# Performance work log

Hardware: AMD Instinct MI355X
Metric: run time of the kernel (lower is better)

The kernel has to match this reference:

```python
import jax, jax.numpy as jnp
import numpy as np

D_MODEL, H, D_FF = 1024, 16, 4096
D_K = D_MODEL // H

def _linear_params(key, fan_in, fan_out):
    kw, kb = jax.random.split(key)
    lim = 1.0 / np.sqrt(fan_in)
    W = jax.random.uniform(kw, (fan_in, fan_out), minval=-lim, maxval=lim, dtype=jnp.float32)
    b = jax.random.uniform(kb, (fan_out,), minval=-lim, maxval=lim, dtype=jnp.float32)
    return W, b

def setup_inputs() -> dict:
    key = jax.random.key(0)
    ks = jax.random.split(key, 8)
    x = jax.random.normal(ks[0], (4, 2048, D_MODEL), dtype=jnp.float32)
    Wq, bq = _linear_params(ks[1], D_MODEL, D_MODEL)
    Wk, bk = _linear_params(ks[2], D_MODEL, D_MODEL)
    Wv, bv = _linear_params(ks[3], D_MODEL, D_MODEL)
    Wo, bo = _linear_params(ks[4], D_MODEL, D_MODEL)
    W1, b1 = _linear_params(ks[5], D_MODEL, D_FF)
    W2, b2 = _linear_params(ks[6], D_FF, D_MODEL)
    g1 = jnp.ones((D_MODEL,), jnp.float32); be1 = jnp.zeros((D_MODEL,), jnp.float32)
    g2 = jnp.ones((D_MODEL,), jnp.float32); be2 = jnp.zeros((D_MODEL,), jnp.float32)
    return {"x": x, "Wq": Wq, "bq": bq, "Wk": Wk, "bk": bk, "Wv": Wv, "bv": bv,
            "Wo": Wo, "bo": bo, "W1": W1, "b1": b1, "W2": W2, "b2": b2,
            "g1": g1, "be1": be1, "g2": g2, "be2": be2}

def _layernorm(x, g, b, eps=1e-5):
    mu = jnp.mean(x, axis=-1, keepdims=True)
    var = jnp.mean(jnp.square(x - mu), axis=-1, keepdims=True)
    return (x - mu) * jax.lax.rsqrt(var + eps) * g + b

def reference(x, Wq, bq, Wk, bk, Wv, bv, Wo, bo, W1, b1, W2, b2, g1, be1, g2, be2):
    B, S, _ = x.shape
    # project and split heads: [B, H, S, D_K]
    q = (x @ Wq + bq).reshape(B, S, H, D_K).transpose(0, 2, 1, 3)
    k = (x @ Wk + bk).reshape(B, S, H, D_K).transpose(0, 2, 1, 3)
    v = (x @ Wv + bv).reshape(B, S, H, D_K).transpose(0, 2, 1, 3)
    scores = jnp.einsum('bhqd,bhkd->bhqk', q, k) / np.sqrt(D_K).astype(np.float32)
    attn = jax.nn.softmax(scores, axis=-1)
    out = jnp.einsum('bhqk,bhkd->bhqd', attn, v)
    out = out.transpose(0, 2, 1, 3).reshape(B, S, D_MODEL)
    attn_out = out @ Wo + bo
    x1 = _layernorm(x + attn_out, g1, be1)
    ffn = jax.nn.relu(x1 @ W1 + b1) @ W2 + b2  # dropout is identity in eval
    return _layernorm(x1 + ffn, g2, be2)
```

## Files before the change

kernel.cpp:

```cpp
#include <hip/hip_runtime.h>

typedef __bf16 bf16;
typedef __bf16 bf16x4 __attribute__((ext_vector_type(4)));
typedef __bf16 bf16x8 __attribute__((ext_vector_type(8)));
typedef float  f32x4  __attribute__((ext_vector_type(4)));

#define DM   1024
#define NH   16
#define DKH  64
#define DFF  4096
#define SEQL 2048
#define NTOK 8192

typedef __attribute__((address_space(1))) void GAS;
typedef __attribute__((address_space(3))) void LAS;

__device__ inline void gload_lds16(const void* g, void* l) {
    __builtin_amdgcn_global_load_lds((GAS*)g, (LAS*)l, 16, 0, 0);
}

__global__ void cast_f32_bf16(const float* __restrict__ in, bf16* __restrict__ out, long n) {
    long i = ((long)blockIdx.x * 256 + threadIdx.x) * 4;
    long stride = (long)gridDim.x * 256 * 4;
    for (; i < n; i += stride) {
        float4 v = *(const float4*)(in + i);
        bf16x4 o = {(bf16)v.x, (bf16)v.y, (bf16)v.z, (bf16)v.w};
        *(bf16x4*)(out + i) = o;
    }
}

__global__ void transpose_cast(const float* __restrict__ src, bf16* __restrict__ dst, int R, int C) {
    __shared__ float t[32][33];
    int c0 = blockIdx.x * 32, r0 = blockIdx.y * 32;
    int tx = threadIdx.x, ty = threadIdx.y;
#pragma unroll
    for (int i = 0; i < 4; ++i)
        t[ty + i * 8][tx] = src[(long)(r0 + ty + i * 8) * C + c0 + tx];
    __syncthreads();
#pragma unroll
    for (int i = 0; i < 4; ++i)
        dst[(long)(c0 + ty + i * 8) * R + r0 + tx] = (bf16)t[tx][ty + i * 8];
}

__global__ void concat3(const float* __restrict__ a, const float* __restrict__ b,
                        const float* __restrict__ c, float* __restrict__ out) {
    int i = blockIdx.x * 256 + threadIdx.x;
    if (i < 1024) out[i] = a[i];
    else if (i < 2048) out[i] = b[i - 1024];
    else if (i < 3072) out[i] = c[i - 2048];
}

__global__ void build_vt(const bf16* __restrict__ qkv, bf16* __restrict__ vt) {
    __shared__ bf16 t[32][33];
    int bh = blockIdx.z, b = bh >> 4, h = bh & 15;
    int s0 = blockIdx.x * 32, d0 = blockIdx.y * 32;
    int tx = threadIdx.x, ty = threadIdx.y;
#pragma unroll
    for (int i = 0; i < 4; ++i)
        t[ty + i * 8][tx] = qkv[(long)(b * SEQL + s0 + ty + i * 8) * 3072 + 2 * DM + h * DKH + d0 + tx];
    __syncthreads();
#pragma unroll
    for (int i = 0; i < 4; ++i)
        vt[((long)bh * DKH + d0 + ty + i * 8) * SEQL + s0 + tx] = (bf16)t[tx][ty + i * 8];
}

__global__ __launch_bounds__(512, 2)
void gemm8p(const bf16* __restrict__ A, const bf16* __restrict__ Bt,
            const float* __restrict__ bias,
            float* __restrict__ Cf, bf16* __restrict__ Ch,
            int N, int lda, int Klen, int relu, long strideCf) {
    __shared__ bf16 As[4][4][256][8];
    __shared__ bf16 Bs[4][4][256][8];
    const int tid = threadIdx.x;
    const int lane = tid & 63;
    const int wv = tid >> 6;
    const int wr = wv >> 2, wc = wv & 3;
    const int lr = lane & 15, lg = lane >> 4;

    unsigned gx = gridDim.x, gy = gridDim.y;
    unsigned nwg = gx * gy * gridDim.z;
    unsigned wg = (blockIdx.z * gy + blockIdx.y) * gx + blockIdx.x;
    unsigned swz = (wg & 7) * (nwg >> 3) + (wg >> 3);
    unsigned bxi = swz % gx;
    unsigned rem = swz / gx;
    unsigned byi = rem % gy, bzi = rem / gy;

    const long brow = (long)byi * 256;
    const long bcol = (long)bxi * 256;
    const bf16* Ap = A + (long)bzi * Klen;
    const bf16* Bp = Bt + (long)bzi * Klen;
    float* Cfp = Cf ? Cf + (long)bzi * strideCf : nullptr;
    const float* biasp = (bzi == 0) ? bias : nullptr;

    auto stageA = [&](int X) {
        const int kt = X * 32, buf = X & 3;
#pragma unroll
        for (int j = 0; j < 2; ++j) {
            int l = j * 512 + tid;
            int kg = l >> 8, row = l & 255;
            gload_lds16(Ap + (brow + row) * (long)lda + kt + kg * 8, &As[buf][kg][row][0]);
        }
    };
    auto stageB = [&](int X) {
        const int kt = X * 32, buf = X & 3;
#pragma unroll
        for (int j = 0; j < 2; ++j) {
            int l = j * 512 + tid;
            int kg = l >> 8, row = l & 255;
            gload_lds16(Bp + (bcol + row) * (long)lda + kt + kg * 8, &Bs[buf][kg][row][0]);
        }
    };

    const int NT = Klen / 32;
    f32x4 acc[8][4] = {};

    for (int p = 0; p < 3 && p < NT; ++p) { stageA(p); stageB(p); }

    for (int T = 0; T < NT; ++T) {
        const int cur = T & 3;
        if (T + 3 < NT) stageA(T + 3);
        if (T + 3 < NT)      asm volatile("s_waitcnt vmcnt(10)" ::: "memory");
        else if (T + 2 < NT) asm volatile("s_waitcnt vmcnt(8)"  ::: "memory");
        else if (T + 1 < NT) asm volatile("s_waitcnt vmcnt(4)"  ::: "memory");
        else                 asm volatile("s_waitcnt vmcnt(0)"  ::: "memory");
        __builtin_amdgcn_s_barrier();
        asm volatile("" ::: "memory");

        bf16x8 bfv[4], af[4];
#pragma unroll
        for (int n = 0; n < 4; ++n)
            bfv[n] = *(const bf16x8*)(&Bs[cur][lg][wc * 64 + n * 16 + lr][0]);
#pragma unroll
        for (int m = 0; m < 4; ++m)
            af[m] = *(const bf16x8*)(&As[cur][lg][wr * 128 + m * 16 + lr][0]);
        asm volatile("s_waitcnt lgkmcnt(0)" ::: "memory");
        __builtin_amdgcn_sched_barrier(0);
        __builtin_amdgcn_s_setprio(1);
#pragma unroll
        for (int m = 0; m < 4; ++m)
#pragma unroll
            for (int n = 0; n < 4; ++n)
                acc[m][n] = __builtin_amdgcn_mfma_f32_16x16x32_bf16(af[m], bfv[n], acc[m][n], 0, 0, 0);
        __builtin_amdgcn_s_setprio(0);

        bf16x8 af2[4];
#pragma unroll
        for (int m = 0; m < 4; ++m)
            af2[m] = *(const bf16x8*)(&As[cur][lg][wr * 128 + (4 + m) * 16 + lr][0]);
        if (T + 3 < NT) stageB(T + 3);
        asm volatile("" ::: "memory");
        __builtin_amdgcn_s_barrier();
        asm volatile("s_waitcnt lgkmcnt(0)" ::: "memory");
        __builtin_amdgcn_sched_barrier(0);
        __builtin_amdgcn_s_setprio(1);
#pragma unroll
        for (int m = 0; m < 4; ++m)
#pragma unroll
            for (int n = 0; n < 4; ++n)
                acc[4 + m][n] = __builtin_amdgcn_mfma_f32_16x16x32_bf16(af2[m], bfv[n], acc[4 + m][n], 0, 0, 0);
        __builtin_amdgcn_s_setprio(0);
        asm volatile("" ::: "memory");
        __builtin_amdgcn_s_barrier();
    }

#pragma unroll
    for (int m = 0; m < 8; ++m) {
#pragma unroll
        for (int n = 0; n < 4; ++n) {
            long gcol = bcol + wc * 64 + n * 16 + lr;
            float bv = biasp ? biasp[gcol] : 0.f;
#pragma unroll
            for (int r = 0; r < 4; ++r) {
                long grow = brow + wr * 128 + m * 16 + lg * 4 + r;
                float v = acc[m][n][r] + bv;
                if (relu) v = v > 0.f ? v : 0.f;
                if (Cfp) Cfp[grow * N + gcol] = v;
                if (Ch) Ch[grow * N + gcol] = (bf16)v;
            }
        }
    }
}

__global__ __launch_bounds__(256, 3)
void attn_fwd(const bf16* __restrict__ qkv, const bf16* __restrict__ vt,
              bf16* __restrict__ attn_o) {
    __shared__ bf16 Ks[2][64][64];
    __shared__ bf16 Vs[2][64][64];
    __shared__ bf16 Plds[4][16][64];
    const int tid = threadIdx.x, lane = tid & 63, w = tid >> 6;
    const int lr = lane & 15, lg = lane >> 4;

    unsigned nwg = gridDim.x * gridDim.y;
    unsigned wg = blockIdx.y * gridDim.x + blockIdx.x;
    unsigned cpx = nwg >> 3;
    unsigned swzid = (wg & 7) * cpx + (wg >> 3);
    const int bx = swzid % gridDim.x, bh = swzid / gridDim.x;
    const int b = bh >> 4, h = bh & 15;
    const int q0 = bx * 128 + w * 32;

    const bf16* Q  = qkv + (long)b * SEQL * 3072 + h * DKH;
    const bf16* Kp = qkv + (long)b * SEQL * 3072 + DM + h * DKH;
    const bf16* Vp = vt + (long)bh * DKH * SEQL;

    const int r0 = w * 8 + (lane >> 3);
    const int cbb = ((lane & 7) * 16) ^ ((r0 & 7) << 4);
    const int cb = cbb >> 1;

    auto stage = [&](int buf, int j0) {
#pragma unroll
        for (int c = 0; c < 2; ++c) {
            bf16* kd = &Ks[buf][0][0] + c * 2048 + w * 512 + lane * 8;
            bf16* vd = &Vs[buf][0][0] + c * 2048 + w * 512 + lane * 8;
            gload_lds16(Kp + (long)(j0 + c * 32 + r0) * 3072 + cb, kd);
            gload_lds16(Vp + (long)(c * 32 + r0) * SEQL + j0 + cb, vd);
        }
    };

    stage(0, 0);

    bf16x8 aq[2][2];
#pragma unroll
    for (int a = 0; a < 2; ++a)
#pragma unroll
        for (int kh = 0; kh < 2; ++kh) {
            bf16x8 q = *(const bf16x8*)(Q + (long)(q0 + a * 16 + lr) * 3072 + kh * 32 + lg * 8);
#pragma unroll
            for (int e = 0; e < 8; ++e) q[e] = (bf16)((float)q[e] * 0.125f);
            aq[a][kh] = q;
        }

    float mrow[2] = {-1e30f, -1e30f};
    float lrow[2] = {0.f, 0.f};
    f32x4 accO[2][4] = {};
    char* pbase = (char*)&Plds[w][0][0];
    const int psw = (lr & 7) << 4;
    const f32x4 zero = {0.f, 0.f, 0.f, 0.f};
    int cur = 0;

    for (int it = 0; it < SEQL / 64; ++it) {
        if (it < SEQL / 64 - 1) {
            stage(cur ^ 1, (it + 1) * 64);
            asm volatile("s_waitcnt vmcnt(4)" ::: "memory");
        } else {
            asm volatile("s_waitcnt vmcnt(0)" ::: "memory");
        }
        __builtin_amdgcn_s_barrier();
        asm volatile("" ::: "memory");

        const char* Kbuf = (const char*)&Ks[cur][0][0];
        const char* Vbuf = (const char*)&Vs[cur][0][0];

        bf16x8 kf[4][2];
#pragma unroll
        for (int jh = 0; jh < 4; ++jh) {
            int row = jh * 16 + lr;
            int sw = (row & 7) << 4;
            kf[jh][0] = *(const bf16x8*)(Kbuf + row * 128 + ((lg * 16) ^ sw));
            kf[jh][1] = *(const bf16x8*)(Kbuf + row * 128 + ((64 + lg * 16) ^ sw));
        }
        bf16x8 vf[4][2];
#pragma unroll
        for (int c = 0; c < 4; ++c) {
            int row = c * 16 + lr;
            int sw = (row & 7) << 4;
            vf[c][0] = *(const bf16x8*)(Vbuf + row * 128 + ((lg * 16) ^ sw));
            vf[c][1] = *(const bf16x8*)(Vbuf + row * 128 + ((64 + lg * 16) ^ sw));
        }

#pragma unroll
        for (int a = 0; a < 2; ++a) {
            f32x4 s[4];
#pragma unroll
            for (int jh = 0; jh < 4; ++jh) {
                f32x4 t = __builtin_amdgcn_mfma_f32_16x16x32_bf16(kf[jh][0], aq[a][0], zero, 0, 0, 0);
                s[jh] = __builtin_amdgcn_mfma_f32_16x16x32_bf16(kf[jh][1], aq[a][1], t, 0, 0, 0);
            }
            float pm = s[0][0];
#pragma unroll
            for (int jh = 0; jh < 4; ++jh)
#pragma unroll
                for (int r = 0; r < 4; ++r) pm = fmaxf(pm, s[jh][r]);
            pm = fmaxf(pm, __shfl_xor(pm, 16));
            pm = fmaxf(pm, __shfl_xor(pm, 32));
            float mnew = fmaxf(mrow[a], pm);
            float al = __expf(mrow[a] - mnew);
            mrow[a] = mnew;
            float psum = 0.f;
#pragma unroll
            for (int jh = 0; jh < 4; ++jh)
#pragma unroll
                for (int r = 0; r < 4; ++r) {
                    float p = __expf(s[jh][r] - mnew);
                    s[jh][r] = p;
                    psum += p;
                }
            psum += __shfl_xor(psum, 16);
            psum += __shfl_xor(psum, 32);
            lrow[a] = lrow[a] * al + psum;
#pragma unroll
            for (int jh = 0; jh < 4; ++jh) {
                bf16x4 pw = {(bf16)s[jh][0], (bf16)s[jh][1], (bf16)s[jh][2], (bf16)s[jh][3]};
                *(bf16x4*)(pbase + lr * 128 + ((jh * 32 + lg * 8) ^ psw)) = pw;
            }
            float alr[4];
#pragma unroll
            for (int r = 0; r < 4; ++r)
                alr[r] = __shfl(al, (lane & 48) | (lg * 4 + r));
#pragma unroll
            for (int c = 0; c < 4; ++c)
#pragma unroll
                for (int r = 0; r < 4; ++r) accO[a][c][r] *= alr[r];
            bf16x8 pa[2];
#pragma unroll
            for (int i = 0; i < 2; ++i)
                pa[i] = *(const bf16x8*)(pbase + lr * 128 + ((i * 64 + lg * 16) ^ psw));
#pragma unroll
            for (int c = 0; c < 4; ++c) {
                accO[a][c] = __builtin_amdgcn_mfma_f32_16x16x32_bf16(pa[0], vf[c][0], accO[a][c], 0, 0, 0);
                accO[a][c] = __builtin_amdgcn_mfma_f32_16x16x32_bf16(pa[1], vf[c][1], accO[a][c], 0, 0, 0);
            }
        }
        asm volatile("" ::: "memory");
        __builtin_amdgcn_s_barrier();
        cur ^= 1;
    }

#pragma unroll
    for (int a = 0; a < 2; ++a) {
        float linv = 1.0f / lrow[a];
        float invr[4];
#pragma unroll
        for (int r = 0; r < 4; ++r)
            invr[r] = __shfl(linv, (lane & 48) | (lg * 4 + r));
#pragma unroll
        for (int r = 0; r < 4; ++r) {
            long grow = (long)b * SEQL + q0 + a * 16 + lg * 4 + r;
#pragma unroll
            for (int c = 0; c < 4; ++c)
                attn_o[grow * DM + h * DKH + c * 16 + lr] = (bf16)(accO[a][c][r] * invr[r]);
        }
    }
}

__global__ __launch_bounds__(256)
void add_ln(const float* __restrict__ A, const float* __restrict__ B,
            const float* __restrict__ B2,
            const float* __restrict__ g, const float* __restrict__ be,
            float* __restrict__ outf, bf16* __restrict__ outh) {
    const int w = threadIdx.x >> 6, lane = threadIdx.x & 63;
    const long row = (long)blockIdx.x * 4 + w;
    const float4* pa = (const float4*)(A + row * DM);
    const float4* pb = (const float4*)(B + row * DM);
    const float4* pb2 = B2 ? (const float4*)(B2 + row * DM) : nullptr;
    float4 v[4];
    float s = 0.f;
#pragma unroll
    for (int i = 0; i < 4; ++i) {
        float4 a = pa[i * 64 + lane], bb = pb[i * 64 + lane];
        v[i] = make_float4(a.x + bb.x, a.y + bb.y, a.z + bb.z, a.w + bb.w);
        if (pb2) {
            float4 b2 = pb2[i * 64 + lane];
            v[i].x += b2.x; v[i].y += b2.y; v[i].z += b2.z; v[i].w += b2.w;
        }
        s += v[i].x + v[i].y + v[i].z + v[i].w;
    }
#pragma unroll
    for (int off = 32; off; off >>= 1) s += __shfl_xor(s, off);
    float mu = s * (1.0f / 1024.0f);
    float var = 0.f;
#pragma unroll
    for (int i = 0; i < 4; ++i) {
        float dx = v[i].x - mu, dy = v[i].y - mu, dz = v[i].z - mu, dw = v[i].w - mu;
        var += dx * dx + dy * dy + dz * dz + dw * dw;
    }
#pragma unroll
    for (int off = 32; off; off >>= 1) var += __shfl_xor(var, off);
    float rs = 1.0f / sqrtf(var * (1.0f / 1024.0f) + 1e-5f);
    const float4* pg = (const float4*)g;
    const float4* pe = (const float4*)be;
#pragma unroll
    for (int i = 0; i < 4; ++i) {
        float4 gg = pg[i * 64 + lane], ee = pe[i * 64 + lane];
        float4 o = make_float4((v[i].x - mu) * rs * gg.x + ee.x,
                               (v[i].y - mu) * rs * gg.y + ee.y,
                               (v[i].z - mu) * rs * gg.z + ee.z,
                               (v[i].w - mu) * rs * gg.w + ee.w);
        if (outf) ((float4*)(outf + row * DM))[i * 64 + lane] = o;
        if (outh) {
            bf16x4 ho = {(bf16)o.x, (bf16)o.y, (bf16)o.z, (bf16)o.w};
            *(bf16x4*)(outh + row * DM + (i * 64 + lane) * 4) = ho;
        }
    }
}

extern "C" void kernel_launch(void* const* d_in, const int* in_sizes, int n_in,
                              void* d_out, int out_size, void* d_ws, size_t ws_size,
                              hipStream_t stream) {
    const float* x   = (const float*)d_in[0];
    const float* Wq  = (const float*)d_in[1];
    const float* bq  = (const float*)d_in[2];
    const float* Wk  = (const float*)d_in[3];
    const float* bk  = (const float*)d_in[4];
    const float* Wv  = (const float*)d_in[5];
    const float* bv  = (const float*)d_in[6];
    const float* Wo  = (const float*)d_in[7];
    const float* bo  = (const float*)d_in[8];
    const float* W1  = (const float*)d_in[9];
    const float* b1  = (const float*)d_in[10];
    const float* W2  = (const float*)d_in[11];
    const float* b2  = (const float*)d_in[12];
    const float* g1  = (const float*)d_in[13];
    const float* be1 = (const float*)d_in[14];
    const float* g2  = (const float*)d_in[15];
    const float* be2 = (const float*)d_in[16];
    float* out = (float*)d_out;

    char* ws = (char*)d_ws;
    size_t off = 0;
    auto alloc = [&](size_t bytes) {
        void* p = ws + off;
        off += (bytes + 255) & ~(size_t)255;
        return p;
    };
    bf16* xh    = (bf16*)alloc((size_t)NTOK * DM * 2);
    bf16* wqkvt = (bf16*)alloc((size_t)3072 * 1024 * 2);
    bf16* wot   = (bf16*)alloc((size_t)1024 * 1024 * 2);
    bf16* w1t   = (bf16*)alloc((size_t)4096 * 1024 * 2);
    bf16* w2t   = (bf16*)alloc((size_t)1024 * 4096 * 2);
    float* bqkv = (float*)alloc((size_t)3072 * 4);
    bf16* qkv   = (bf16*)alloc((size_t)NTOK * 3072 * 2);
    bf16* vtb   = (bf16*)alloc((size_t)NTOK * DM * 2);
    bf16* attno = (bf16*)alloc((size_t)NTOK * DM * 2);
    float* projf  = (float*)alloc((size_t)NTOK * DM * 4);
    float* projf1 = (float*)alloc((size_t)NTOK * DM * 4);
    float* x1f  = (float*)alloc((size_t)NTOK * DM * 4);
    bf16* x1h   = (bf16*)alloc((size_t)NTOK * DM * 2);
    bf16* ffh   = (bf16*)qkv;

    dim3 tb(32, 8);
    cast_f32_bf16<<<2048, 256, 0, stream>>>(x, xh, (long)NTOK * DM);
    transpose_cast<<<dim3(32, 32), tb, 0, stream>>>(Wq, wqkvt, 1024, 1024);
    transpose_cast<<<dim3(32, 32), tb, 0, stream>>>(Wk, wqkvt + (size_t)1024 * 1024, 1024, 1024);
    transpose_cast<<<dim3(32, 32), tb, 0, stream>>>(Wv, wqkvt + (size_t)2048 * 1024, 1024, 1024);
    transpose_cast<<<dim3(32, 32), tb, 0, stream>>>(Wo, wot, 1024, 1024);
    transpose_cast<<<dim3(128, 32), tb, 0, stream>>>(W1, w1t, 1024, 4096);
    transpose_cast<<<dim3(32, 128), tb, 0, stream>>>(W2, w2t, 4096, 1024);
    concat3<<<12, 256, 0, stream>>>(bq, bk, bv, bqkv);

    gemm8p<<<dim3(3072 / 256, 8192 / 256, 1), 512, 0, stream>>>(
        xh, wqkvt, bqkv, nullptr, qkv, 3072, 1024, 1024, 0, 0);
    build_vt<<<dim3(SEQL / 32, 2, 64), tb, 0, stream>>>(qkv, vtb);
    attn_fwd<<<dim3(SEQL / 128, 64), 256, 0, stream>>>(qkv, vtb, attno);
    gemm8p<<<dim3(1024 / 256, 8192 / 256, 2), 512, 0, stream>>>(
        attno, wot, bo, projf, nullptr, 1024, 1024, 512, 0, (long)NTOK * DM);
    add_ln<<<NTOK / 4, 256, 0, stream>>>(x, projf, projf1, g1, be1, x1f, x1h);
    gemm8p<<<dim3(4096 / 256, 8192 / 256, 1), 512, 0, stream>>>(
        x1h, w1t, b1, nullptr, ffh, 4096, 1024, 1024, 1, 0);
    gemm8p<<<dim3(1024 / 256, 8192 / 256, 2), 512, 0, stream>>>(
        ffh, w2t, b2, projf, nullptr, 1024, 4096, 2048, 0, (long)NTOK * DM);
    add_ln<<<NTOK / 4, 256, 0, stream>>>(x1f, projf, projf1, g2, be2, out, nullptr);
}
```

Measured before the change: 565.9 us.

## Interleave GEMM LDS reads with MFMA and restructure attention softmax and LDS layout

The GEMM main loop now loads A fragments in pairs with partial lgkmcnt waits, so MFMAs start before all LDS reads finish, and one of the three per-iteration barriers is removed. The attention kernel switches K/V/P shared memory from XOR-swizzled rows to a k-group-major layout, folds log2(e) into the Q scale so it can use exp2f, and skips the running-max rescale when the new max exceeds the old by at most 8 (in log2 units). Together these aim to cut LDS wait stalls, barrier count and exp/rescale work. The lazy rescale keeps the exact result only while exponentials stay bounded by 2^8, and dropping the swizzle may bring back LDS bank conflicts.

```diff
diff --git a/kernel.cpp b/kernel.cpp
--- a/kernel.cpp
+++ b/kernel.cpp
@@ -82,8 +82,8 @@
     unsigned wg = (blockIdx.z * gy + blockIdx.y) * gx + blockIdx.x;
     unsigned swz = (wg & 7) * (nwg >> 3) + (wg >> 3);
     unsigned bxi = swz % gx;
-    unsigned rem = swz / gx;
-    unsigned byi = rem % gy, bzi = rem / gy;
+    unsigned rem2 = swz / gx;
+    unsigned byi = rem2 % gy, bzi = rem2 / gy;
 
     const long brow = (long)byi * 256;
     const long bcol = (long)bxi * 256;
@@ -126,38 +126,54 @@
         __builtin_amdgcn_s_barrier();
         asm volatile("" ::: "memory");
 
-        bf16x8 bfv[4], af[4];
+        bf16x8 bfv[4], af[8];
 #pragma unroll
         for (int n = 0; n < 4; ++n)
             bfv[n] = *(const bf16x8*)(&Bs[cur][lg][wc * 64 + n * 16 + lr][0]);
-#pragma unroll
-        for (int m = 0; m < 4; ++m)
-            af[m] = *(const bf16x8*)(&As[cur][lg][wr * 128 + m * 16 + lr][0]);
+        af[0] = *(const bf16x8*)(&As[cur][lg][wr * 128 + 0 * 16 + lr][0]);
+        af[1] = *(const bf16x8*)(&As[cur][lg][wr * 128 + 1 * 16 + lr][0]);
+        af[2] = *(const bf16x8*)(&As[cur][lg][wr * 128 + 2 * 16 + lr][0]);
+        af[3] = *(const bf16x8*)(&As[cur][lg][wr * 128 + 3 * 16 + lr][0]);
+        asm volatile("s_waitcnt lgkmcnt(2)" ::: "memory");
+        __builtin_amdgcn_sched_barrier(0);
+        __builtin_amdgcn_s_setprio(1);
+#pragma unroll
+        for (int mm = 0; mm < 2; ++mm)
+#pragma unroll
+            for (int n = 0; n < 4; ++n)
+                acc[mm][n] = __builtin_amdgcn_mfma_f32_16x16x32_bf16(af[mm], bfv[n], acc[mm][n], 0, 0, 0);
+        __builtin_amdgcn_s_setprio(0);
+        af[4] = *(const bf16x8*)(&As[cur][lg][wr * 128 + 4 * 16 + lr][0]);
+        af[5] = *(const bf16x8*)(&As[cur][lg][wr * 128 + 5 * 16 + lr][0]);
+        asm volatile("s_waitcnt lgkmcnt(2)" ::: "memory");
+        __builtin_amdgcn_sched_barrier(0);
+        __builtin_amdgcn_s_setprio(1);
+#pragma unroll
+        for (int mm = 2; mm < 4; ++mm)
+#pragma unroll
+            for (int n = 0; n < 4; ++n)
+                acc[mm][n] = __builtin_amdgcn_mfma_f32_16x16x32_bf16(af[mm], bfv[n], acc[mm][n], 0, 0, 0);
+        __builtin_amdgcn_s_setprio(0);
+        af[6] = *(const bf16x8*)(&As[cur][lg][wr * 128 + 6 * 16 + lr][0]);
+        af[7] = *(const bf16x8*)(&As[cur][lg][wr * 128 + 7 * 16 + lr][0]);
+        if (T + 3 < NT) stageB(T + 3);
+        asm volatile("s_waitcnt lgkmcnt(2)" ::: "memory");
+        __builtin_amdgcn_sched_barrier(0);
+        __builtin_amdgcn_s_setprio(1);
+#pragma unroll
+        for (int mm = 4; mm < 6; ++mm)
+#pragma unroll
+            for (int n = 0; n < 4; ++n)
+                acc[mm][n] = __builtin_amdgcn_mfma_f32_16x16x32_bf16(af[mm], bfv[n], acc[mm][n], 0, 0, 0);
+        __builtin_amdgcn_s_setprio(0);
         asm volatile("s_waitcnt lgkmcnt(0)" ::: "memory");
         __builtin_amdgcn_sched_barrier(0);
         __builtin_amdgcn_s_setprio(1);
 #pragma unroll
-        for (int m = 0; m < 4; ++m)
+        for (int mm = 6; mm < 8; ++mm)
 #pragma unroll
             for (int n = 0; n < 4; ++n)
-                acc[m][n] = __builtin_amdgcn_mfma_f32_16x16x32_bf16(af[m], bfv[n], acc[m][n], 0, 0, 0);
-        __builtin_amdgcn_s_setprio(0);
-
-        bf16x8 af2[4];
-#pragma unroll
-        for (int m = 0; m < 4; ++m)
-            af2[m] = *(const bf16x8*)(&As[cur][lg][wr * 128 + (4 + m) * 16 + lr][0]);
-        if (T + 3 < NT) stageB(T + 3);
-        asm volatile("" ::: "memory");
-        __builtin_amdgcn_s_barrier();
-        asm volatile("s_waitcnt lgkmcnt(0)" ::: "memory");
-        __builtin_amdgcn_sched_barrier(0);
-        __builtin_amdgcn_s_setprio(1);
-#pragma unroll
-        for (int m = 0; m < 4; ++m)
-#pragma unroll
-            for (int n = 0; n < 4; ++n)
-                acc[4 + m][n] = __builtin_amdgcn_mfma_f32_16x16x32_bf16(af2[m], bfv[n], acc[4 + m][n], 0, 0, 0);
+                acc[mm][n] = __builtin_amdgcn_mfma_f32_16x16x32_bf16(af[mm], bfv[n], acc[mm][n], 0, 0, 0);
         __builtin_amdgcn_s_setprio(0);
         asm volatile("" ::: "memory");
         __builtin_amdgcn_s_barrier();
@@ -184,9 +200,9 @@
 __global__ __launch_bounds__(256, 3)
 void attn_fwd(const bf16* __restrict__ qkv, const bf16* __restrict__ vt,
               bf16* __restrict__ attn_o) {
-    __shared__ bf16 Ks[2][64][64];
-    __shared__ bf16 Vs[2][64][64];
-    __shared__ bf16 Plds[4][16][64];
+    __shared__ bf16 Ks[2][8][64][8];
+    __shared__ bf16 Vs[2][8][64][8];
+    __shared__ bf16 Plds[4][8][16][8];
     const int tid = threadIdx.x, lane = tid & 63, w = tid >> 6;
     const int lr = lane & 15, lg = lane >> 4;
 
@@ -202,22 +218,19 @@
     const bf16* Kp = qkv + (long)b * SEQL * 3072 + DM + h * DKH;
     const bf16* Vp = vt + (long)bh * DKH * SEQL;
 
-    const int r0 = w * 8 + (lane >> 3);
-    const int cbb = ((lane & 7) * 16) ^ ((r0 & 7) << 4);
-    const int cb = cbb >> 1;
-
     auto stage = [&](int buf, int j0) {
 #pragma unroll
         for (int c = 0; c < 2; ++c) {
-            bf16* kd = &Ks[buf][0][0] + c * 2048 + w * 512 + lane * 8;
-            bf16* vd = &Vs[buf][0][0] + c * 2048 + w * 512 + lane * 8;
-            gload_lds16(Kp + (long)(j0 + c * 32 + r0) * 3072 + cb, kd);
-            gload_lds16(Vp + (long)(c * 32 + r0) * SEQL + j0 + cb, vd);
+            int idx = c * 256 + tid;
+            int kg = idx >> 6, row = idx & 63;
+            gload_lds16(Kp + (long)(j0 + row) * 3072 + kg * 8, &Ks[buf][kg][row][0]);
+            gload_lds16(Vp + (long)row * SEQL + j0 + kg * 8, &Vs[buf][kg][row][0]);
         }
     };
 
     stage(0, 0);
 
+    const float QSC = 0.125f * 1.44269504f;
     bf16x8 aq[2][2];
 #pragma unroll
     for (int a = 0; a < 2; ++a)
@@ -225,15 +238,13 @@
         for (int kh = 0; kh < 2; ++kh) {
             bf16x8 q = *(const bf16x8*)(Q + (long)(q0 + a * 16 + lr) * 3072 + kh * 32 + lg * 8);
 #pragma unroll
-            for (int e = 0; e < 8; ++e) q[e] = (bf16)((float)q[e] * 0.125f);
+            for (int e = 0; e < 8; ++e) q[e] = (bf16)((float)q[e] * QSC);
             aq[a][kh] = q;
         }
 
     float mrow[2] = {-1e30f, -1e30f};
     float lrow[2] = {0.f, 0.f};
     f32x4 accO[2][4] = {};
-    char* pbase = (char*)&Plds[w][0][0];
-    const int psw = (lr & 7) << 4;
     const f32x4 zero = {0.f, 0.f, 0.f, 0.f};
     int cur = 0;
 
@@ -247,25 +258,18 @@
         __builtin_amdgcn_s_barrier();
         asm volatile("" ::: "memory");
 
-        const char* Kbuf = (const char*)&Ks[cur][0][0];
-        const char* Vbuf = (const char*)&Vs[cur][0][0];
-
         bf16x8 kf[4][2];
 #pragma unroll
-        for (int jh = 0; jh < 4; ++jh) {
-            int row = jh * 16 + lr;
-            int sw = (row & 7) << 4;
-            kf[jh][0] = *(const bf16x8*)(Kbuf + row * 128 + ((lg * 16) ^ sw));
-            kf[jh][1] = *(const bf16x8*)(Kbuf + row * 128 + ((64 + lg * 16) ^ sw));
-        }
+        for (int jh = 0; jh < 4; ++jh)
+#pragma unroll
+            for (int kh = 0; kh < 2; ++kh)
+                kf[jh][kh] = *(const bf16x8*)(&Ks[cur][kh * 4 + lg][jh * 16 + lr][0]);
         bf16x8 vf[4][2];
 #pragma unroll
-        for (int c = 0; c < 4; ++c) {
-            int row = c * 16 + lr;
-            int sw = (row & 7) << 4;
-            vf[c][0] = *(const bf16x8*)(Vbuf + row * 128 + ((lg * 16) ^ sw));
-            vf[c][1] = *(const bf16x8*)(Vbuf + row * 128 + ((64 + lg * 16) ^ sw));
-        }
+        for (int c = 0; c < 4; ++c)
+#pragma unroll
+            for (int kh = 0; kh < 2; ++kh)
+                vf[c][kh] = *(const bf16x8*)(&Vs[cur][kh * 4 + lg][c * 16 + lr][0]);
 
 #pragma unroll
         for (int a = 0; a < 2; ++a) {
@@ -282,15 +286,16 @@
                 for (int r = 0; r < 4; ++r) pm = fmaxf(pm, s[jh][r]);
             pm = fmaxf(pm, __shfl_xor(pm, 16));
             pm = fmaxf(pm, __shfl_xor(pm, 32));
-            float mnew = fmaxf(mrow[a], pm);
-            float al = __expf(mrow[a] - mnew);
-            mrow[a] = mnew;
+            int skip = __all(pm <= mrow[a] + 8.0f);
+            float mnew, al;
+            if (skip) { mnew = mrow[a]; al = 1.0f; }
+            else { mnew = fmaxf(mrow[a], pm); al = exp2f(mrow[a] - mnew); mrow[a] = mnew; }
             float psum = 0.f;
 #pragma unroll
             for (int jh = 0; jh < 4; ++jh)
 #pragma unroll
                 for (int r = 0; r < 4; ++r) {
-                    float p = __expf(s[jh][r] - mnew);
+                    float p = exp2f(s[jh][r] - mnew);
                     s[jh][r] = p;
                     psum += p;
                 }
@@ -300,20 +305,22 @@
 #pragma unroll
             for (int jh = 0; jh < 4; ++jh) {
                 bf16x4 pw = {(bf16)s[jh][0], (bf16)s[jh][1], (bf16)s[jh][2], (bf16)s[jh][3]};
-                *(bf16x4*)(pbase + lr * 128 + ((jh * 32 + lg * 8) ^ psw)) = pw;
+                *(bf16x4*)(&Plds[w][jh * 2 + (lg >> 1)][lr][(lg & 1) * 4]) = pw;
             }
-            float alr[4];
-#pragma unroll
-            for (int r = 0; r < 4; ++r)
-                alr[r] = __shfl(al, (lane & 48) | (lg * 4 + r));
-#pragma unroll
-            for (int c = 0; c < 4; ++c)
-#pragma unroll
-                for (int r = 0; r < 4; ++r) accO[a][c][r] *= alr[r];
+            if (!skip) {
+                float alr[4];
+#pragma unroll
+                for (int r = 0; r < 4; ++r)
+                    alr[r] = __shfl(al, (lane & 48) | (lg * 4 + r));
+#pragma unroll
+                for (int c = 0; c < 4; ++c)
+#pragma unroll
+                    for (int r = 0; r < 4; ++r) accO[a][c][r] *= alr[r];
+            }
             bf16x8 pa[2];
 #pragma unroll
             for (int i = 0; i < 2; ++i)
-                pa[i] = *(const bf16x8*)(pbase + lr * 128 + ((i * 64 + lg * 16) ^ psw));
+                pa[i] = *(const bf16x8*)(&Plds[w][i * 4 + lg][lr][0]);
 #pragma unroll
             for (int c = 0; c < 4; ++c) {
                 accO[a][c] = __builtin_amdgcn_mfma_f32_16x16x32_bf16(pa[0], vf[c][0], accO[a][c], 0, 0, 0);
```

Measured after the change: 589.9 us. 1.04x slower.
